# Performance work log

Measured on AMD Instinct MI355X. Metric: run time of the kernel, lower is better.

Reference implementation:

```python
import jax, jax.numpy as jnp
import numpy as np

B, S, D_IN, H = 64, 512, 2, 512


def lstm_cell(x, h, c, Wih, Whh, b):
    # PyTorch nn.LSTM gate layout: [i, f, g, o] stacked along rows of W (4H x in)
    gates = x @ Wih.T + h @ Whh.T + b  # [B, 4H]
    i, f, g, o = jnp.split(gates, 4, axis=-1)
    c = jax.nn.sigmoid(f) * c + jax.nn.sigmoid(i) * jnp.tanh(g)
    h = jax.nn.sigmoid(o) * jnp.tanh(c)
    return h, c


def setup_inputs() -> dict:
    key = jax.random.key(0)
    ks = jax.random.split(key, 12)
    s = 1.0 / np.sqrt(H)  # torch default uniform init scale
    u = lambda k, shape: jax.random.uniform(k, shape, jnp.float32, -s, s)
    return {
        "inputs": jax.random.normal(ks[0], (B, S, D_IN), jnp.float32),
        "enc_Wih": u(ks[1], (4 * H, D_IN)),
        "enc_Whh": u(ks[2], (4 * H, H)),
        "enc_bih": u(ks[3], (4 * H,)),
        "enc_bhh": u(ks[4], (4 * H,)),
        "dec_Wih": u(ks[5], (4 * H, H)),
        "dec_Whh": u(ks[6], (4 * H, H)),
        "dec_bih": u(ks[7], (4 * H,)),
        "dec_bhh": u(ks[8], (4 * H,)),
        "W_key": u(ks[9], (H, H)),
        "W_query": u(ks[10], (H, H)),
        "v": u(ks[11], (H,)),
        "max_output_len": S,
    }


def reference(inputs, enc_Wih, enc_Whh, enc_bih, enc_bhh,
              dec_Wih, dec_Whh, dec_bih, dec_bhh,
              W_key, W_query, v, max_output_len):
    batch, seq_len, _ = inputs.shape
    hid = W_key.shape[0]
    dtype = inputs.dtype

    # ---- Encoder LSTM over the sequence ----
    enc_b = enc_bih + enc_bhh
    h0 = jnp.zeros((batch, hid), dtype)

    def enc_step(carry, x_t):
        h, c = carry
        h, c = lstm_cell(x_t, h, c, enc_Wih, enc_Whh, enc_b)
        return (h, c), h

    (h, c), enc_outs = jax.lax.scan(enc_step, (h0, h0), jnp.swapaxes(inputs, 0, 1))
    enc_outs = jnp.swapaxes(enc_outs, 0, 1)  # [B, S, H]

    # keys are recomputed each step in the torch code but are step-invariant
    keys = enc_outs @ W_key.T  # [B, S, H]
    dec_b = dec_bih + dec_bhh

    # ---- Decoder loop with Bahdanau pointer attention ----
    def dec_step(carry, _):
        h_d, c_d, x = carry
        h_d, c_d = lstm_cell(x, h_d, c_d, dec_Wih, dec_Whh, dec_b)
        query = h_d @ W_query.T                                # [B, H]
        scores = jnp.tanh(query[:, None, :] + keys) @ v        # [B, S]
        probs = jax.nn.softmax(scores, axis=-1)
        context = jnp.einsum('bs,bsh->bh', probs, enc_outs)    # [B, H]
        return (h_d, c_d, context), scores

    x0 = jnp.zeros((batch, hid), dtype)
    _, all_scores = jax.lax.scan(dec_step, (h, c, x0), None, length=max_output_len)
    return jnp.swapaxes(all_scores, 0, 1)  # [B, T, S]
```

## Files before the change

kernel.cpp:

```cpp
#include <hip/hip_runtime.h>

constexpr int kNB = 64;
constexpr int kNS = 512;
constexpr int kNH = 512;
constexpr int kNG = 2048;
constexpr int kNT = 512;

__device__ __forceinline__ float chpn_sigmoid(float x) {
    return 1.0f / (1.0f + __expf(-x));
}
__device__ __forceinline__ float chpn_tanh(float x) {
    x = fmaxf(fminf(x, 15.0f), -15.0f);
    float e = __expf(2.0f * x);
    return (e - 1.0f) / (e + 1.0f);
}

__global__ void ConvexHullPointerNetwork_57303453663418_kernel(
    const float* ebih, const float* ebhh,
    const float* dbih, const float* dbhh,
    const float* wq,
    float* enc_b, float* dec_b, float* wqT, float* h0c)
{
    int i = blockIdx.x * 256 + threadIdx.x;
    if (i < kNG) { enc_b[i] = ebih[i] + ebhh[i]; dec_b[i] = dbih[i] + dbhh[i]; }
    if (i < 2 * kNB * kNH) h0c[i] = 0.0f;
    if (i < kNH * kNH) {
        int r = i >> 9, c = i & 511;
        wqT[c * kNH + r] = wq[i];
    }
}

__global__ __launch_bounds__(256) void chpn_enc_cell(
    const float* __restrict__ inputs, const float* __restrict__ wih,
    const float* __restrict__ whh, const float* __restrict__ bias,
    const float* __restrict__ h_src, float* __restrict__ h_dst,
    float* __restrict__ c_st, float* __restrict__ enc_outs, int t)
{
    __shared__ float tile[64][65];
    __shared__ float gate_lds[4][64];
    const int tid = threadIdx.x;
    const int bb = tid & 63, gg = tid >> 6;
    const int j = (int)blockIdx.x;

    const int r = gg * kNH + j;
    const float* w = whh + (size_t)r * kNH;
    float acc = 0.f;

    for (int ch = 0; ch < 8; ++ch) {
        const int k0 = ch * 64;
        for (int i = 0; i < 16; ++i) {
            int e = tid + i * 256; int kk = e & 63, b2 = e >> 6;
            tile[kk][b2] = h_src[b2 * kNH + k0 + kk];
        }
        __syncthreads();
        #pragma unroll
        for (int kk = 0; kk < 64; ++kk)
            acc = fmaf(tile[kk][bb], w[k0 + kk], acc);
        __syncthreads();
    }
    float x0 = inputs[(bb * kNS + t) * 2 + 0];
    float x1 = inputs[(bb * kNS + t) * 2 + 1];
    acc += bias[r] + wih[r * 2] * x0 + wih[r * 2 + 1] * x1;

    gate_lds[gg][bb] = acc;
    __syncthreads();
    if (tid < 64) {
        float gi = gate_lds[0][tid], gf = gate_lds[1][tid];
        float gc = gate_lds[2][tid], go = gate_lds[3][tid];
        float cc = chpn_sigmoid(gf) * c_st[tid * kNH + j] + chpn_sigmoid(gi) * chpn_tanh(gc);
        float hh = chpn_sigmoid(go) * chpn_tanh(cc);
        c_st[tid * kNH + j] = cc;
        h_dst[tid * kNH + j] = hh;
        enc_outs[((size_t)tid * kNS + t) * kNH + j] = hh;
    }
}

__global__ __launch_bounds__(256) void chpn_keys_gemm(
    const float* __restrict__ enc_outs, const float* __restrict__ wk,
    float* __restrict__ keysT)
{
    int bid = blockIdx.x;
    int bb = bid >> 6, ht = (bid >> 3) & 7, st = bid & 7;
    __shared__ float asb[32][66];
    __shared__ float bsb[32][66];
    int tid = threadIdx.x;
    int tx = tid & 15, ty = tid >> 4;
    float acc[4][4] = {};
    for (int j0 = 0; j0 < kNH; j0 += 32) {
        for (int i = 0; i < 8; ++i) {
            int e = tid + i * 256;
            int j = e & 31, s = e >> 5;
            asb[j][s] = enc_outs[((size_t)bb * kNS + st * 64 + s) * kNH + j0 + j];
            bsb[j][s] = wk[(size_t)(ht * 64 + s) * kNH + j0 + j];
        }
        __syncthreads();
        #pragma unroll 8
        for (int j = 0; j < 32; ++j) {
            float a0 = asb[j][tx*4], a1 = asb[j][tx*4+1], a2 = asb[j][tx*4+2], a3 = asb[j][tx*4+3];
            float b0 = bsb[j][ty*4], b1 = bsb[j][ty*4+1], b2 = bsb[j][ty*4+2], b3 = bsb[j][ty*4+3];
            acc[0][0] = fmaf(b0,a0,acc[0][0]); acc[0][1] = fmaf(b0,a1,acc[0][1]);
            acc[0][2] = fmaf(b0,a2,acc[0][2]); acc[0][3] = fmaf(b0,a3,acc[0][3]);
            acc[1][0] = fmaf(b1,a0,acc[1][0]); acc[1][1] = fmaf(b1,a1,acc[1][1]);
            acc[1][2] = fmaf(b1,a2,acc[1][2]); acc[1][3] = fmaf(b1,a3,acc[1][3]);
            acc[2][0] = fmaf(b2,a0,acc[2][0]); acc[2][1] = fmaf(b2,a1,acc[2][1]);
            acc[2][2] = fmaf(b2,a2,acc[2][2]); acc[2][3] = fmaf(b2,a3,acc[2][3]);
            acc[3][0] = fmaf(b3,a0,acc[3][0]); acc[3][1] = fmaf(b3,a1,acc[3][1]);
            acc[3][2] = fmaf(b3,a2,acc[3][2]); acc[3][3] = fmaf(b3,a3,acc[3][3]);
        }
        __syncthreads();
    }
    for (int i = 0; i < 4; ++i)
        for (int k = 0; k < 4; ++k)
            keysT[((size_t)bb * kNH + ht * 64 + ty * 4 + i) * kNS + st * 64 + tx * 4 + k] =
                acc[i][k];
}

__global__ __launch_bounds__(256) void chpn_dec_cell(
    const float* __restrict__ wih, const float* __restrict__ whh,
    const float* __restrict__ bias,
    const float* __restrict__ h_src, float* __restrict__ h_dst,
    float* __restrict__ c_st,
    const float* __restrict__ ctx_num, const float* __restrict__ denom,
    int first)
{
    __shared__ float tile[64][65];
    __shared__ float gate_lds[4][64];
    __shared__ float invd[64];
    const int tid = threadIdx.x;
    const int bb = tid & 63, gg = tid >> 6;
    const int j = (int)blockIdx.x;
    if (tid < 64) invd[tid] = first ? 0.0f : (1.0f / denom[tid]);
    __syncthreads();

    const int r = gg * kNH + j;
    float acc = 0.f;
    {
        const float* w = wih + (size_t)r * kNH;
        for (int ch = 0; ch < 8; ++ch) {
            const int k0 = ch * 64;
            for (int i = 0; i < 16; ++i) {
                int e = tid + i * 256; int kk = e & 63, b2 = e >> 6;
                tile[kk][b2] = first ? 0.0f : ctx_num[b2 * kNH + k0 + kk] * invd[b2];
            }
            __syncthreads();
            #pragma unroll
            for (int kk = 0; kk < 64; ++kk)
                acc = fmaf(tile[kk][bb], w[k0 + kk], acc);
            __syncthreads();
        }
    }
    {
        const float* w = whh + (size_t)r * kNH;
        for (int ch = 0; ch < 8; ++ch) {
            const int k0 = ch * 64;
            for (int i = 0; i < 16; ++i) {
                int e = tid + i * 256; int kk = e & 63, b2 = e >> 6;
                tile[kk][b2] = h_src[b2 * kNH + k0 + kk];
            }
            __syncthreads();
            #pragma unroll
            for (int kk = 0; kk < 64; ++kk)
                acc = fmaf(tile[kk][bb], w[k0 + kk], acc);
            __syncthreads();
        }
    }
    acc += bias[r];
    gate_lds[gg][bb] = acc;
    __syncthreads();
    if (tid < 64) {
        float gi = gate_lds[0][tid], gf = gate_lds[1][tid];
        float gc = gate_lds[2][tid], go = gate_lds[3][tid];
        float cc = chpn_sigmoid(gf) * c_st[tid * kNH + j] + chpn_sigmoid(gi) * chpn_tanh(gc);
        float hh = chpn_sigmoid(go) * chpn_tanh(cc);
        c_st[tid * kNH + j] = cc;
        h_dst[tid * kNH + j] = hh;
    }
}

__global__ __launch_bounds__(256) void chpn_query(
    const float* __restrict__ wqT, const float* __restrict__ h_src,
    float* __restrict__ query, float* __restrict__ ctx_num,
    float* __restrict__ denom)
{
    __shared__ float hl[kNH];
    __shared__ float part[256];
    int bid = blockIdx.x;
    int bb = bid >> 2, hc = bid & 3;
    int tid = threadIdx.x;
    int hl_idx = tid;
    hl[hl_idx] = h_src[bb * kNH + hl_idx];
    hl[hl_idx + 256] = h_src[bb * kNH + hl_idx + 256];
    __syncthreads();

    int h = hc * 128 + (tid & 127);
    int jh = tid >> 7;
    float acc = 0.f;
    const float* wcol = wqT + h;
    #pragma unroll 8
    for (int j = jh * 256; j < jh * 256 + 256; ++j)
        acc = fmaf(hl[j], wcol[(size_t)j * kNH], acc);
    part[tid] = acc;
    __syncthreads();
    if (tid < 128) {
        float q = part[tid] + part[tid + 128];
        query[bb * kNH + h] = q;
        ctx_num[bb * kNH + h] = 0.0f;
        if (hc == 0 && tid == 0) denom[bb] = 0.0f;
    }
}

__global__ __launch_bounds__(1024) void chpn_score_ctx(
    const float* __restrict__ keysT, const float* __restrict__ enc_outs,
    const float* __restrict__ query, const float* __restrict__ vvec,
    float* __restrict__ ctx_num, float* __restrict__ denom,
    float* __restrict__ out, int t)
{
    __shared__ float ql[kNH], vl[kNH];
    __shared__ float part[16][64];
    __shared__ float el[64];
    int bid = blockIdx.x;
    int bb = bid >> 3, sc = bid & 7;
    int s0 = sc * 64;
    int tid = threadIdx.x;
    int s = tid & 63, hq = tid >> 6;

    if (tid < kNH) { ql[tid] = query[bb * kNH + tid]; vl[tid] = vvec[tid]; }
    __syncthreads();

    float acc = 0.f;
    const float* kp = keysT + (size_t)bb * kNH * kNS + s0 + s;
    const int h0 = hq * 32;
    #pragma unroll 4
    for (int h = h0; h < h0 + 32; ++h) {
        float kv = kp[(size_t)h * kNS];
        acc = fmaf(vl[h], chpn_tanh(ql[h] + kv), acc);
    }
    part[hq][s] = acc;
    __syncthreads();

    if (tid < 64) {
        float scv = 0.f;
        #pragma unroll
        for (int q = 0; q < 16; ++q) scv += part[q][tid];
        out[((size_t)bb * kNT + t) * kNS + s0 + tid] = scv;
        float e = __expf(scv);
        el[tid] = e;
        float wsum = e;
        #pragma unroll
        for (int off = 32; off > 0; off >>= 1) wsum += __shfl_down(wsum, off);
        if (tid == 0) atomicAdd(&denom[bb], wsum);
    }
    __syncthreads();

    int j = tid & 511, sh = tid >> 9;
    float a = 0.f;
    const float* ep = enc_outs + ((size_t)bb * kNS + s0 + sh * 32) * kNH + j;
    #pragma unroll 4
    for (int ss = 0; ss < 32; ++ss)
        a = fmaf(el[sh * 32 + ss], ep[(size_t)ss * kNH], a);
    atomicAdd(&ctx_num[bb * kNH + j], a);
}

extern "C" void kernel_launch(void* const* d_in, const int* in_sizes, int n_in,
                              void* d_out, int out_size, void* d_ws, size_t ws_size,
                              hipStream_t stream) {
    const float* inputs = (const float*)d_in[0];
    const float* e_wih  = (const float*)d_in[1];
    const float* e_whh  = (const float*)d_in[2];
    const float* e_bih  = (const float*)d_in[3];
    const float* e_bhh  = (const float*)d_in[4];
    const float* d_wih  = (const float*)d_in[5];
    const float* d_whh  = (const float*)d_in[6];
    const float* d_bih  = (const float*)d_in[7];
    const float* d_bhh  = (const float*)d_in[8];
    const float* w_key  = (const float*)d_in[9];
    const float* w_qry  = (const float*)d_in[10];
    const float* v_vec  = (const float*)d_in[11];
    float* out = (float*)d_out;

    float* wsf   = (float*)d_ws;
    float* h0    = wsf;
    float* cst   = h0 + kNB * kNH;
    float* h1    = cst + kNB * kNH;
    float* query = h1 + kNB * kNH;
    float* ctxn  = query + kNB * kNH;
    float* denom = ctxn + kNB * kNH;
    float* encb  = denom + 64;
    float* decb  = encb + kNG;
    float* wqT   = decb + kNG;
    float* keysF = wqT + (size_t)kNH * kNH;
    float* encF  = keysF + (size_t)kNB * kNH * kNS;

    ConvexHullPointerNetwork_57303453663418_kernel<<<1024, 256, 0, stream>>>(
        e_bih, e_bhh, d_bih, d_bhh, w_qry, encb, decb, wqT, h0);

    for (int t = 0; t < kNS; ++t) {
        float* hs = (t & 1) ? h1 : h0;
        float* hd = (t & 1) ? h0 : h1;
        chpn_enc_cell<<<512, 256, 0, stream>>>(inputs, e_wih, e_whh, encb,
                                               hs, hd, cst, encF, t);
    }

    chpn_keys_gemm<<<4096, 256, 0, stream>>>(encF, w_key, keysF);

    for (int t = 0; t < kNT; ++t) {
        float* hs = (t & 1) ? h1 : h0;
        float* hd = (t & 1) ? h0 : h1;
        chpn_dec_cell<<<512, 256, 0, stream>>>(d_wih, d_whh, decb,
                                               hs, hd, cst,
                                               ctxn, denom, t == 0 ? 1 : 0);
        chpn_query<<<256, 256, 0, stream>>>(wqT, hd, query, ctxn, denom);
        chpn_score_ctx<<<512, 1024, 0, stream>>>(keysF, encF, query, v_vec,
                                                 ctxn, denom, out, t);
    }
}
```

Before: 70.88 ms.

## Replace per-step kernel launches with persistent cooperative kernels using grid sync

Encoder and decoder recurrences now each run as a single cooperative persistent kernel of 256 blocks x 512 threads. Each block handles two hidden units, and steps are separated by grid.sync() instead of about 2000 separate kernel launches. The decoder fuses the LSTM cell, query projection and score/context stages into one loop with three grid barriers per step. Score and context work is remapped to 128-position chunks per block. This removes launch overhead but lowers parallelism per stage (256 blocks instead of 512 for the attention step) and adds grid-wide barrier cost. The old multi-launch path is kept as a fallback if the cooperative launch fails.

```diff
diff --git a/kernel.cpp b/kernel.cpp
--- a/kernel.cpp
+++ b/kernel.cpp
@@ -1,4 +1,7 @@
 #include <hip/hip_runtime.h>
+#include <hip/hip_cooperative_groups.h>
+
+namespace cg = cooperative_groups;
 
 constexpr int kNB = 64;
 constexpr int kNS = 512;
@@ -30,7 +33,205 @@
     }
 }
 
-__global__ __launch_bounds__(256) void chpn_enc_cell(
+__global__ __launch_bounds__(512) void chpn_enc_loop(
+    const float* __restrict__ inputs, const float* __restrict__ wih,
+    const float* __restrict__ whh, const float* __restrict__ bias,
+    float* __restrict__ h0, float* __restrict__ h1,
+    float* __restrict__ c_st, float* __restrict__ enc_outs)
+{
+    cg::grid_group grid = cg::this_grid();
+    __shared__ float tile[64][65];
+    __shared__ float gate_lds[2][4][64];
+    const int tid = threadIdx.x;
+    const int bb = tid & 63, gg = (tid >> 6) & 3, jj = tid >> 8;
+    const int j = (int)blockIdx.x * 2 + jj;
+    const int r = gg * kNH + j;
+    const float* w = whh + (size_t)r * kNH;
+    const float wx0 = wih[r * 2], wx1 = wih[r * 2 + 1], bj = bias[r];
+
+    for (int t = 0; t < kNS; ++t) {
+        const float* hs = (t & 1) ? h1 : h0;
+        float* hd = (t & 1) ? h0 : h1;
+        float acc = 0.f;
+        for (int ch = 0; ch < 8; ++ch) {
+            const int k0 = ch * 64;
+            for (int i = 0; i < 8; ++i) {
+                int e = tid + i * 512; int kk = e & 63, b2 = e >> 6;
+                tile[kk][b2] = hs[b2 * kNH + k0 + kk];
+            }
+            __syncthreads();
+            #pragma unroll
+            for (int kk = 0; kk < 64; ++kk)
+                acc = fmaf(tile[kk][bb], w[k0 + kk], acc);
+            __syncthreads();
+        }
+        float x0 = inputs[(bb * kNS + t) * 2 + 0];
+        float x1 = inputs[(bb * kNS + t) * 2 + 1];
+        acc += bj + wx0 * x0 + wx1 * x1;
+        gate_lds[jj][gg][bb] = acc;
+        __syncthreads();
+        if (tid < 128) {
+            int j2 = (int)blockIdx.x * 2 + (tid >> 6), b = tid & 63;
+            int jl = tid >> 6;
+            float gi = gate_lds[jl][0][b], gf = gate_lds[jl][1][b];
+            float gc = gate_lds[jl][2][b], go = gate_lds[jl][3][b];
+            float cc = chpn_sigmoid(gf) * c_st[b * kNH + j2] +
+                       chpn_sigmoid(gi) * chpn_tanh(gc);
+            float hh = chpn_sigmoid(go) * chpn_tanh(cc);
+            c_st[b * kNH + j2] = cc;
+            hd[b * kNH + j2] = hh;
+            enc_outs[((size_t)b * kNS + t) * kNH + j2] = hh;
+        }
+        __syncthreads();
+        grid.sync();
+    }
+}
+
+__global__ __launch_bounds__(512) void chpn_dec_loop(
+    const float* __restrict__ wih, const float* __restrict__ whh,
+    const float* __restrict__ bias, const float* __restrict__ wqT,
+    const float* __restrict__ vvec,
+    const float* __restrict__ keysT, const float* __restrict__ enc_outs,
+    float* __restrict__ h0, float* __restrict__ h1, float* __restrict__ c_st,
+    float* __restrict__ query, float* __restrict__ ctx_num,
+    float* __restrict__ denom, float* __restrict__ out)
+{
+    cg::grid_group grid = cg::this_grid();
+    __shared__ float tile[64][65];
+    __shared__ float gate_lds[2][4][64];
+    __shared__ float invd[64];
+    __shared__ float qpart[4][128];
+    __shared__ float ql[kNH], vl[kNH];
+    __shared__ float part[4][128];
+    __shared__ float el[128];
+
+    const int tid = threadIdx.x;
+    const int bid = (int)blockIdx.x;
+    const int bb = tid & 63, gg = (tid >> 6) & 3, jj = tid >> 8;
+    const int j = bid * 2 + jj;
+    const int rr = gg * kNH + j;
+    const float* wih_r = wih + (size_t)rr * kNH;
+    const float* whh_r = whh + (size_t)rr * kNH;
+    const float bias_r = bias[rr];
+    const int qb = bid >> 2, qc = bid & 3;
+    const int s0 = qc * 128;
+
+    for (int t = 0; t < kNT; ++t) {
+        const int first = (t == 0);
+        const float* hs = (t & 1) ? h1 : h0;
+        float* hd = (t & 1) ? h0 : h1;
+
+        if (tid < 64) invd[tid] = first ? 0.0f : (1.0f / denom[tid]);
+        __syncthreads();
+        float acc = 0.f;
+        for (int ch = 0; ch < 8; ++ch) {
+            const int k0 = ch * 64;
+            for (int i = 0; i < 8; ++i) {
+                int e = tid + i * 512; int kk = e & 63, b2 = e >> 6;
+                tile[kk][b2] = first ? 0.0f
+                             : ctx_num[b2 * kNH + k0 + kk] * invd[b2];
+            }
+            __syncthreads();
+            #pragma unroll
+            for (int kk = 0; kk < 64; ++kk)
+                acc = fmaf(tile[kk][bb], wih_r[k0 + kk], acc);
+            __syncthreads();
+        }
+        for (int ch = 0; ch < 8; ++ch) {
+            const int k0 = ch * 64;
+            for (int i = 0; i < 8; ++i) {
+                int e = tid + i * 512; int kk = e & 63, b2 = e >> 6;
+                tile[kk][b2] = hs[b2 * kNH + k0 + kk];
+            }
+            __syncthreads();
+            #pragma unroll
+            for (int kk = 0; kk < 64; ++kk)
+                acc = fmaf(tile[kk][bb], whh_r[k0 + kk], acc);
+            __syncthreads();
+        }
+        acc += bias_r;
+        gate_lds[jj][gg][bb] = acc;
+        __syncthreads();
+        if (tid < 128) {
+            int j2 = bid * 2 + (tid >> 6), b = tid & 63;
+            int jl = tid >> 6;
+            float gi = gate_lds[jl][0][b], gf = gate_lds[jl][1][b];
+            float gc = gate_lds[jl][2][b], go = gate_lds[jl][3][b];
+            float cc = chpn_sigmoid(gf) * c_st[b * kNH + j2] +
+                       chpn_sigmoid(gi) * chpn_tanh(gc);
+            float hh = chpn_sigmoid(go) * chpn_tanh(cc);
+            c_st[b * kNH + j2] = cc;
+            hd[b * kNH + j2] = hh;
+        }
+        __syncthreads();
+        grid.sync();
+
+        {
+            int h = qc * 128 + (tid & 127);
+            int jq = tid >> 7;
+            float qa = 0.f;
+            const float* wcol = wqT + h;
+            const float* hb = hd + qb * kNH;
+            #pragma unroll 8
+            for (int jx = jq * 128; jx < jq * 128 + 128; ++jx)
+                qa = fmaf(hb[jx], wcol[(size_t)jx * kNH], qa);
+            qpart[jq][tid & 127] = qa;
+            __syncthreads();
+            if (tid < 128) {
+                float q = qpart[0][tid] + qpart[1][tid] +
+                          qpart[2][tid] + qpart[3][tid];
+                query[qb * kNH + qc * 128 + tid] = q;
+                ctx_num[qb * kNH + qc * 128 + tid] = 0.0f;
+                if (qc == 0 && tid == 0) denom[qb] = 0.0f;
+            }
+            __syncthreads();
+        }
+        grid.sync();
+
+        {
+            ql[tid] = query[qb * kNH + tid];
+            vl[tid] = vvec[tid];
+            __syncthreads();
+
+            int s = tid & 127, hq = tid >> 7;
+            float sa = 0.f;
+            const float* kp = keysT + (size_t)qb * kNH * kNS + s0 + s;
+            const int h0i = hq * 128;
+            #pragma unroll 4
+            for (int h = h0i; h < h0i + 128; ++h) {
+                float kv = kp[(size_t)h * kNS];
+                sa = fmaf(vl[h], chpn_tanh(ql[h] + kv), sa);
+            }
+            part[hq][s] = sa;
+            __syncthreads();
+
+            if (tid < 128) {
+                float scv = part[0][tid] + part[1][tid] +
+                            part[2][tid] + part[3][tid];
+                out[((size_t)qb * kNT + t) * kNS + s0 + tid] = scv;
+                float e = __expf(scv);
+                el[tid] = e;
+                float wsum = e;
+                #pragma unroll
+                for (int off = 32; off > 0; off >>= 1)
+                    wsum += __shfl_down(wsum, off);
+                if ((tid & 63) == 0) atomicAdd(&denom[qb], wsum);
+            }
+            __syncthreads();
+
+            float a = 0.f;
+            const float* ep = enc_outs + ((size_t)qb * kNS + s0) * kNH + tid;
+            #pragma unroll 4
+            for (int ss = 0; ss < 128; ++ss)
+                a = fmaf(el[ss], ep[(size_t)ss * kNH], a);
+            atomicAdd(&ctx_num[qb * kNH + tid], a);
+            __syncthreads();
+        }
+        grid.sync();
+    }
+}
+
+__global__ __launch_bounds__(256) void fb_enc_cell(
     const float* __restrict__ inputs, const float* __restrict__ wih,
     const float* __restrict__ whh, const float* __restrict__ bias,
     const float* __restrict__ h_src, float* __restrict__ h_dst,
@@ -41,11 +242,9 @@
     const int tid = threadIdx.x;
     const int bb = tid & 63, gg = tid >> 6;
     const int j = (int)blockIdx.x;
-
     const int r = gg * kNH + j;
     const float* w = whh + (size_t)r * kNH;
     float acc = 0.f;
-
     for (int ch = 0; ch < 8; ++ch) {
         const int k0 = ch * 64;
         for (int i = 0; i < 16; ++i) {
@@ -61,7 +260,6 @@
     float x0 = inputs[(bb * kNS + t) * 2 + 0];
     float x1 = inputs[(bb * kNS + t) * 2 + 1];
     acc += bias[r] + wih[r * 2] * x0 + wih[r * 2 + 1] * x1;
-
     gate_lds[gg][bb] = acc;
     __syncthreads();
     if (tid < 64) {
@@ -73,6 +271,145 @@
         h_dst[tid * kNH + j] = hh;
         enc_outs[((size_t)tid * kNS + t) * kNH + j] = hh;
     }
+}
+
+__global__ __launch_bounds__(256) void fb_dec_cell(
+    const float* __restrict__ wih, const float* __restrict__ whh,
+    const float* __restrict__ bias,
+    const float* __restrict__ h_src, float* __restrict__ h_dst,
+    float* __restrict__ c_st,
+    const float* __restrict__ ctx_num, const float* __restrict__ denom,
+    int first)
+{
+    __shared__ float tile[64][65];
+    __shared__ float gate_lds[4][64];
+    __shared__ float invd[64];
+    const int tid = threadIdx.x;
+    const int bb = tid & 63, gg = tid >> 6;
+    const int j = (int)blockIdx.x;
+    if (tid < 64) invd[tid] = first ? 0.0f : (1.0f / denom[tid]);
+    __syncthreads();
+    const int r = gg * kNH + j;
+    float acc = 0.f;
+    {
+        const float* w = wih + (size_t)r * kNH;
+        for (int ch = 0; ch < 8; ++ch) {
+            const int k0 = ch * 64;
+            for (int i = 0; i < 16; ++i) {
+                int e = tid + i * 256; int kk = e & 63, b2 = e >> 6;
+                tile[kk][b2] = first ? 0.0f : ctx_num[b2 * kNH + k0 + kk] * invd[b2];
+            }
+            __syncthreads();
+            #pragma unroll
+            for (int kk = 0; kk < 64; ++kk)
+                acc = fmaf(tile[kk][bb], w[k0 + kk], acc);
+            __syncthreads();
+        }
+    }
+    {
+        const float* w = whh + (size_t)r * kNH;
+        for (int ch = 0; ch < 8; ++ch) {
+            const int k0 = ch * 64;
+            for (int i = 0; i < 16; ++i) {
+                int e = tid + i * 256; int kk = e & 63, b2 = e >> 6;
+                tile[kk][b2] = h_src[b2 * kNH + k0 + kk];
+            }
+            __syncthreads();
+            #pragma unroll
+            for (int kk = 0; kk < 64; ++kk)
+                acc = fmaf(tile[kk][bb], w[k0 + kk], acc);
+            __syncthreads();
+        }
+    }
+    acc += bias[r];
+    gate_lds[gg][bb] = acc;
+    __syncthreads();
+    if (tid < 64) {
+        float gi = gate_lds[0][tid], gf = gate_lds[1][tid];
+        float gc = gate_lds[2][tid], go = gate_lds[3][tid];
+        float cc = chpn_sigmoid(gf) * c_st[tid * kNH + j] + chpn_sigmoid(gi) * chpn_tanh(gc);
+        float hh = chpn_sigmoid(go) * chpn_tanh(cc);
+        c_st[tid * kNH + j] = cc;
+        h_dst[tid * kNH + j] = hh;
+    }
+}
+
+__global__ __launch_bounds__(256) void fb_query(
+    const float* __restrict__ wqT, const float* __restrict__ h_src,
+    float* __restrict__ query, float* __restrict__ ctx_num,
+    float* __restrict__ denom)
+{
+    __shared__ float hl[kNH];
+    __shared__ float partq[256];
+    int bid = blockIdx.x;
+    int bb = bid >> 2, hc = bid & 3;
+    int tid = threadIdx.x;
+    hl[tid] = h_src[bb * kNH + tid];
+    hl[tid + 256] = h_src[bb * kNH + tid + 256];
+    __syncthreads();
+    int h = hc * 128 + (tid & 127);
+    int jh = tid >> 7;
+    float acc = 0.f;
+    const float* wcol = wqT + h;
+    #pragma unroll 8
+    for (int j = jh * 256; j < jh * 256 + 256; ++j)
+        acc = fmaf(hl[j], wcol[(size_t)j * kNH], acc);
+    partq[tid] = acc;
+    __syncthreads();
+    if (tid < 128) {
+        float q = partq[tid] + partq[tid + 128];
+        query[bb * kNH + h] = q;
+        ctx_num[bb * kNH + h] = 0.0f;
+        if (hc == 0 && tid == 0) denom[bb] = 0.0f;
+    }
+}
+
+__global__ __launch_bounds__(1024) void fb_score_ctx(
+    const float* __restrict__ keysT, const float* __restrict__ enc_outs,
+    const float* __restrict__ query, const float* __restrict__ vvec,
+    float* __restrict__ ctx_num, float* __restrict__ denom,
+    float* __restrict__ out, int t)
+{
+    __shared__ float ql[kNH], vl[kNH];
+    __shared__ float part[16][64];
+    __shared__ float el[64];
+    int bid = blockIdx.x;
+    int bb = bid >> 3, sc = bid & 7;
+    int s0 = sc * 64;
+    int tid = threadIdx.x;
+    int s = tid & 63, hq = tid >> 6;
+    if (tid < kNH) { ql[tid] = query[bb * kNH + tid]; vl[tid] = vvec[tid]; }
+    __syncthreads();
+    float acc = 0.f;
+    const float* kp = keysT + (size_t)bb * kNH * kNS + s0 + s;
+    const int h0 = hq * 32;
+    #pragma unroll 4
+    for (int h = h0; h < h0 + 32; ++h) {
+        float kv = kp[(size_t)h * kNS];
+        acc = fmaf(vl[h], chpn_tanh(ql[h] + kv), acc);
+    }
+    part[hq][s] = acc;
+    __syncthreads();
+    if (tid < 64) {
+        float scv = 0.f;
+        #pragma unroll
+        for (int q = 0; q < 16; ++q) scv += part[q][tid];
+        out[((size_t)bb * kNT + t) * kNS + s0 + tid] = scv;
+        float e = __expf(scv);
+        el[tid] = e;
+        float wsum = e;
+        #pragma unroll
+        for (int off = 32; off > 0; off >>= 1) wsum += __shfl_down(wsum, off);
+        if (tid == 0) atomicAdd(&denom[bb], wsum);
+    }
+    __syncthreads();
+    int j = tid & 511, sh = tid >> 9;
+    float a = 0.f;
+    const float* ep = enc_outs + ((size_t)bb * kNS + s0 + sh * 32) * kNH + j;
+    #pragma unroll 4
+    for (int ss = 0; ss < 32; ++ss)
+        a = fmaf(el[sh * 32 + ss], ep[(size_t)ss * kNH], a);
+    atomicAdd(&ctx_num[bb * kNH + j], a);
 }
 
 __global__ __launch_bounds__(256) void chpn_keys_gemm(
@@ -113,152 +450,6 @@
         for (int k = 0; k < 4; ++k)
             keysT[((size_t)bb * kNH + ht * 64 + ty * 4 + i) * kNS + st * 64 + tx * 4 + k] =
                 acc[i][k];
-}
-
-__global__ __launch_bounds__(256) void chpn_dec_cell(
-    const float* __restrict__ wih, const float* __restrict__ whh,
-    const float* __restrict__ bias,
-    const float* __restrict__ h_src, float* __restrict__ h_dst,
-    float* __restrict__ c_st,
-    const float* __restrict__ ctx_num, const float* __restrict__ denom,
-    int first)
-{
-    __shared__ float tile[64][65];
-    __shared__ float gate_lds[4][64];
-    __shared__ float invd[64];
-    const int tid = threadIdx.x;
-    const int bb = tid & 63, gg = tid >> 6;
-    const int j = (int)blockIdx.x;
-    if (tid < 64) invd[tid] = first ? 0.0f : (1.0f / denom[tid]);
-    __syncthreads();
-
-    const int r = gg * kNH + j;
-    float acc = 0.f;
-    {
-        const float* w = wih + (size_t)r * kNH;
-        for (int ch = 0; ch < 8; ++ch) {
-            const int k0 = ch * 64;
-            for (int i = 0; i < 16; ++i) {
-                int e = tid + i * 256; int kk = e & 63, b2 = e >> 6;
-                tile[kk][b2] = first ? 0.0f : ctx_num[b2 * kNH + k0 + kk] * invd[b2];
-            }
-            __syncthreads();
-            #pragma unroll
-            for (int kk = 0; kk < 64; ++kk)
-                acc = fmaf(tile[kk][bb], w[k0 + kk], acc);
-            __syncthreads();
-        }
-    }
-    {
-        const float* w = whh + (size_t)r * kNH;
-        for (int ch = 0; ch < 8; ++ch) {
-            const int k0 = ch * 64;
-            for (int i = 0; i < 16; ++i) {
-                int e = tid + i * 256; int kk = e & 63, b2 = e >> 6;
-                tile[kk][b2] = h_src[b2 * kNH + k0 + kk];
-            }
-            __syncthreads();
-            #pragma unroll
-            for (int kk = 0; kk < 64; ++kk)
-                acc = fmaf(tile[kk][bb], w[k0 + kk], acc);
-            __syncthreads();
-        }
-    }
-    acc += bias[r];
-    gate_lds[gg][bb] = acc;
-    __syncthreads();
-    if (tid < 64) {
-        float gi = gate_lds[0][tid], gf = gate_lds[1][tid];
-        float gc = gate_lds[2][tid], go = gate_lds[3][tid];
-        float cc = chpn_sigmoid(gf) * c_st[tid * kNH + j] + chpn_sigmoid(gi) * chpn_tanh(gc);
-        float hh = chpn_sigmoid(go) * chpn_tanh(cc);
-        c_st[tid * kNH + j] = cc;
-        h_dst[tid * kNH + j] = hh;
-    }
-}
-
-__global__ __launch_bounds__(256) void chpn_query(
-    const float* __restrict__ wqT, const float* __restrict__ h_src,
-    float* __restrict__ query, float* __restrict__ ctx_num,
-    float* __restrict__ denom)
-{
-    __shared__ float hl[kNH];
-    __shared__ float part[256];
-    int bid = blockIdx.x;
-    int bb = bid >> 2, hc = bid & 3;
-    int tid = threadIdx.x;
-    int hl_idx = tid;
-    hl[hl_idx] = h_src[bb * kNH + hl_idx];
-    hl[hl_idx + 256] = h_src[bb * kNH + hl_idx + 256];
-    __syncthreads();
-
-    int h = hc * 128 + (tid & 127);
-    int jh = tid >> 7;
-    float acc = 0.f;
-    const float* wcol = wqT + h;
-    #pragma unroll 8
-    for (int j = jh * 256; j < jh * 256 + 256; ++j)
-        acc = fmaf(hl[j], wcol[(size_t)j * kNH], acc);
-    part[tid] = acc;
-    __syncthreads();
-    if (tid < 128) {
-        float q = part[tid] + part[tid + 128];
-        query[bb * kNH + h] = q;
-        ctx_num[bb * kNH + h] = 0.0f;
-        if (hc == 0 && tid == 0) denom[bb] = 0.0f;
-    }
-}
-
-__global__ __launch_bounds__(1024) void chpn_score_ctx(
-    const float* __restrict__ keysT, const float* __restrict__ enc_outs,
-    const float* __restrict__ query, const float* __restrict__ vvec,
-    float* __restrict__ ctx_num, float* __restrict__ denom,
-    float* __restrict__ out, int t)
-{
-    __shared__ float ql[kNH], vl[kNH];
-    __shared__ float part[16][64];
-    __shared__ float el[64];
-    int bid = blockIdx.x;
-    int bb = bid >> 3, sc = bid & 7;
-    int s0 = sc * 64;
-    int tid = threadIdx.x;
-    int s = tid & 63, hq = tid >> 6;
-
-    if (tid < kNH) { ql[tid] = query[bb * kNH + tid]; vl[tid] = vvec[tid]; }
-    __syncthreads();
-
-    float acc = 0.f;
-    const float* kp = keysT + (size_t)bb * kNH * kNS + s0 + s;
-    const int h0 = hq * 32;
-    #pragma unroll 4
-    for (int h = h0; h < h0 + 32; ++h) {
-        float kv = kp[(size_t)h * kNS];
-        acc = fmaf(vl[h], chpn_tanh(ql[h] + kv), acc);
-    }
-    part[hq][s] = acc;
-    __syncthreads();
-
-    if (tid < 64) {
-        float scv = 0.f;
-        #pragma unroll
-        for (int q = 0; q < 16; ++q) scv += part[q][tid];
-        out[((size_t)bb * kNT + t) * kNS + s0 + tid] = scv;
-        float e = __expf(scv);
-        el[tid] = e;
-        float wsum = e;
-        #pragma unroll
-        for (int off = 32; off > 0; off >>= 1) wsum += __shfl_down(wsum, off);
-        if (tid == 0) atomicAdd(&denom[bb], wsum);
-    }
-    __syncthreads();
-
-    int j = tid & 511, sh = tid >> 9;
-    float a = 0.f;
-    const float* ep = enc_outs + ((size_t)bb * kNS + s0 + sh * 32) * kNH + j;
-    #pragma unroll 4
-    for (int ss = 0; ss < 32; ++ss)
-        a = fmaf(el[sh * 32 + ss], ep[(size_t)ss * kNH], a);
-    atomicAdd(&ctx_num[bb * kNH + j], a);
 }
 
 extern "C" void kernel_launch(void* const* d_in, const int* in_sizes, int n_in,
@@ -294,23 +485,47 @@
     ConvexHullPointerNetwork_57303453663418_kernel<<<1024, 256, 0, stream>>>(
         e_bih, e_bhh, d_bih, d_bhh, w_qry, encb, decb, wqT, h0);
 
-    for (int t = 0; t < kNS; ++t) {
-        float* hs = (t & 1) ? h1 : h0;
-        float* hd = (t & 1) ? h0 : h1;
-        chpn_enc_cell<<<512, 256, 0, stream>>>(inputs, e_wih, e_whh, encb,
-                                               hs, hd, cst, encF, t);
+    {
+        void* args[] = { (void*)&inputs, (void*)&e_wih, (void*)&e_whh,
+                         (void*)&encb, (void*)&h0, (void*)&h1,
+                         (void*)&cst, (void*)&encF };
+        hipError_t rc = hipLaunchCooperativeKernel((const void*)chpn_enc_loop,
+                                                   dim3(256), dim3(512),
+                                                   args, 0, stream);
+        if (rc != hipSuccess) {
+            (void)hipGetLastError();
+            for (int t = 0; t < kNS; ++t) {
+                float* hs = (t & 1) ? h1 : h0;
+                float* hd = (t & 1) ? h0 : h1;
+                fb_enc_cell<<<512, 256, 0, stream>>>(inputs, e_wih, e_whh, encb,
+                                                     hs, hd, cst, encF, t);
+            }
+        }
     }
 
     chpn_keys_gemm<<<4096, 256, 0, stream>>>(encF, w_key, keysF);
 
-    for (int t = 0; t < kNT; ++t) {
-        float* hs = (t & 1) ? h1 : h0;
-        float* hd = (t & 1) ? h0 : h1;
-        chpn_dec_cell<<<512, 256, 0, stream>>>(d_wih, d_whh, decb,
-                                               hs, hd, cst,
-                                               ctxn, denom, t == 0 ? 1 : 0);
-        chpn_query<<<256, 256, 0, stream>>>(wqT, hd, query, ctxn, denom);
-        chpn_score_ctx<<<512, 1024, 0, stream>>>(keysF, encF, query, v_vec,
-                                                 ctxn, denom, out, t);
-    }
-}
+    {
+        void* args[] = { (void*)&d_wih, (void*)&d_whh, (void*)&decb,
+                         (void*)&wqT, (void*)&v_vec, (void*)&keysF,
+                         (void*)&encF, (void*)&h0, (void*)&h1, (void*)&cst,
+                         (void*)&query, (void*)&ctxn, (void*)&denom,
+                         (void*)&out };
+        hipError_t rc = hipLaunchCooperativeKernel((const void*)chpn_dec_loop,
+                                                   dim3(256), dim3(512),
+                                                   args, 0, stream);
+        if (rc != hipSuccess) {
+            (void)hipGetLastError();
+            for (int t = 0; t < kNT; ++t) {
+                float* hs = (t & 1) ? h1 : h0;
+                float* hd = (t & 1) ? h0 : h1;
+                fb_dec_cell<<<512, 256, 0, stream>>>(d_wih, d_whh, decb,
+                                                     hs, hd, cst,
+                                                     ctxn, denom, t == 0 ? 1 : 0);
+                fb_query<<<256, 256, 0, stream>>>(wqT, hd, query, ctxn, denom);
+                fb_score_ctx<<<512, 1024, 0, stream>>>(keysF, encF, query, v_vec,
+                                                       ctxn, denom, out, t);
+            }
+        }
+    }
+}
```

Result: slower. 127.8 ms (+80.3%).

## Store encoder outputs and keys in fp16 and restructure query projection

Applied to the files above, without the earlier changes.

Encoder outputs and the precomputed attention keys are now stored as _Float16 instead of float. This halves the memory traffic of the per-step score/context kernel, which streams keys and encoder outputs for the whole batch every decoder step. The query projection is also rewritten to read W_query rows directly, with an LDS-staged hidden tile shared across the batch, so the W_query transpose in the setup kernel is dropped. The cost is reduced precision in the keys and encoder outputs, which feed the output scores and the context vector.

```diff
diff --git a/kernel.cpp b/kernel.cpp
--- a/kernel.cpp
+++ b/kernel.cpp
@@ -6,6 +6,8 @@
 constexpr int kNG = 2048;
 constexpr int kNT = 512;
 
+typedef _Float16 chpn_f16;
+
 __device__ __forceinline__ float chpn_sigmoid(float x) {
     return 1.0f / (1.0f + __expf(-x));
 }
@@ -18,34 +20,27 @@
 __global__ void ConvexHullPointerNetwork_57303453663418_kernel(
     const float* ebih, const float* ebhh,
     const float* dbih, const float* dbhh,
-    const float* wq,
-    float* enc_b, float* dec_b, float* wqT, float* h0c)
+    float* enc_b, float* dec_b, float* h0c)
 {
     int i = blockIdx.x * 256 + threadIdx.x;
     if (i < kNG) { enc_b[i] = ebih[i] + ebhh[i]; dec_b[i] = dbih[i] + dbhh[i]; }
     if (i < 2 * kNB * kNH) h0c[i] = 0.0f;
-    if (i < kNH * kNH) {
-        int r = i >> 9, c = i & 511;
-        wqT[c * kNH + r] = wq[i];
-    }
 }
 
 __global__ __launch_bounds__(256) void chpn_enc_cell(
     const float* __restrict__ inputs, const float* __restrict__ wih,
     const float* __restrict__ whh, const float* __restrict__ bias,
     const float* __restrict__ h_src, float* __restrict__ h_dst,
-    float* __restrict__ c_st, float* __restrict__ enc_outs, int t)
+    float* __restrict__ c_st, chpn_f16* __restrict__ enc_outs, int t)
 {
     __shared__ float tile[64][65];
     __shared__ float gate_lds[4][64];
     const int tid = threadIdx.x;
     const int bb = tid & 63, gg = tid >> 6;
     const int j = (int)blockIdx.x;
-
     const int r = gg * kNH + j;
     const float* w = whh + (size_t)r * kNH;
     float acc = 0.f;
-
     for (int ch = 0; ch < 8; ++ch) {
         const int k0 = ch * 64;
         for (int i = 0; i < 16; ++i) {
@@ -61,7 +56,6 @@
     float x0 = inputs[(bb * kNS + t) * 2 + 0];
     float x1 = inputs[(bb * kNS + t) * 2 + 1];
     acc += bias[r] + wih[r * 2] * x0 + wih[r * 2 + 1] * x1;
-
     gate_lds[gg][bb] = acc;
     __syncthreads();
     if (tid < 64) {
@@ -71,13 +65,13 @@
         float hh = chpn_sigmoid(go) * chpn_tanh(cc);
         c_st[tid * kNH + j] = cc;
         h_dst[tid * kNH + j] = hh;
-        enc_outs[((size_t)tid * kNS + t) * kNH + j] = hh;
+        enc_outs[((size_t)tid * kNS + t) * kNH + j] = (chpn_f16)hh;
     }
 }
 
 __global__ __launch_bounds__(256) void chpn_keys_gemm(
-    const float* __restrict__ enc_outs, const float* __restrict__ wk,
-    float* __restrict__ keysT)
+    const chpn_f16* __restrict__ enc_outs, const float* __restrict__ wk,
+    chpn_f16* __restrict__ keysT)
 {
     int bid = blockIdx.x;
     int bb = bid >> 6, ht = (bid >> 3) & 7, st = bid & 7;
@@ -90,7 +84,7 @@
         for (int i = 0; i < 8; ++i) {
             int e = tid + i * 256;
             int j = e & 31, s = e >> 5;
-            asb[j][s] = enc_outs[((size_t)bb * kNS + st * 64 + s) * kNH + j0 + j];
+            asb[j][s] = (float)enc_outs[((size_t)bb * kNS + st * 64 + s) * kNH + j0 + j];
             bsb[j][s] = wk[(size_t)(ht * 64 + s) * kNH + j0 + j];
         }
         __syncthreads();
@@ -112,7 +106,7 @@
     for (int i = 0; i < 4; ++i)
         for (int k = 0; k < 4; ++k)
             keysT[((size_t)bb * kNH + ht * 64 + ty * 4 + i) * kNS + st * 64 + tx * 4 + k] =
-                acc[i][k];
+                (chpn_f16)acc[i][k];
 }
 
 __global__ __launch_bounds__(256) void chpn_dec_cell(
@@ -131,7 +125,6 @@
     const int j = (int)blockIdx.x;
     if (tid < 64) invd[tid] = first ? 0.0f : (1.0f / denom[tid]);
     __syncthreads();
-
     const int r = gg * kNH + j;
     float acc = 0.f;
     {
@@ -177,40 +170,51 @@
     }
 }
 
-__global__ __launch_bounds__(256) void chpn_query(
-    const float* __restrict__ wqT, const float* __restrict__ h_src,
+__global__ __launch_bounds__(256) void chpn_query_ws(
+    const float* __restrict__ wq, const float* __restrict__ h_src,
     float* __restrict__ query, float* __restrict__ ctx_num,
     float* __restrict__ denom)
 {
-    __shared__ float hl[kNH];
-    __shared__ float part[256];
-    int bid = blockIdx.x;
-    int bb = bid >> 2, hc = bid & 3;
-    int tid = threadIdx.x;
-    int hl_idx = tid;
-    hl[hl_idx] = h_src[bb * kNH + hl_idx];
-    hl[hl_idx + 256] = h_src[bb * kNH + hl_idx + 256];
-    __syncthreads();
-
-    int h = hc * 128 + (tid & 127);
-    int jh = tid >> 7;
-    float acc = 0.f;
-    const float* wcol = wqT + h;
-    #pragma unroll 8
-    for (int j = jh * 256; j < jh * 256 + 256; ++j)
-        acc = fmaf(hl[j], wcol[(size_t)j * kNH], acc);
-    part[tid] = acc;
+    __shared__ float tile[128][65];
+    __shared__ float qp[4][2][64];
+    const int tid = threadIdx.x;
+    const int bb = tid & 63, p = tid >> 6;
+    const int h0 = (int)blockIdx.x * 2;
+    const float* w0 = wq + (size_t)h0 * kNH;
+    const float* w1 = w0 + kNH;
+
+    float a0 = 0.f, a1 = 0.f;
+    for (int ch = 0; ch < 4; ++ch) {
+        const int j0 = ch * 128;
+        for (int i = 0; i < 32; ++i) {
+            int e = tid + i * 256; int jj = e & 127, b2 = e >> 7;
+            tile[jj][b2] = h_src[b2 * kNH + j0 + jj];
+        }
+        __syncthreads();
+        if (ch == p) {
+            #pragma unroll 4
+            for (int jj = 0; jj < 128; ++jj) {
+                float hv = tile[jj][bb];
+                a0 = fmaf(hv, w0[j0 + jj], a0);
+                a1 = fmaf(hv, w1[j0 + jj], a1);
+            }
+        }
+        __syncthreads();
+    }
+    qp[p][0][bb] = a0;
+    qp[p][1][bb] = a1;
     __syncthreads();
     if (tid < 128) {
-        float q = part[tid] + part[tid + 128];
-        query[bb * kNH + h] = q;
-        ctx_num[bb * kNH + h] = 0.0f;
-        if (hc == 0 && tid == 0) denom[bb] = 0.0f;
+        int b2 = tid & 63, hh = tid >> 6;
+        float q = qp[0][hh][b2] + qp[1][hh][b2] + qp[2][hh][b2] + qp[3][hh][b2];
+        query[b2 * kNH + h0 + hh] = q;
+        ctx_num[b2 * kNH + h0 + hh] = 0.0f;
+        if (blockIdx.x == 0 && hh == 0) denom[b2] = 0.0f;
     }
 }
 
 __global__ __launch_bounds__(1024) void chpn_score_ctx(
-    const float* __restrict__ keysT, const float* __restrict__ enc_outs,
+    const chpn_f16* __restrict__ keysT, const chpn_f16* __restrict__ enc_outs,
     const float* __restrict__ query, const float* __restrict__ vvec,
     float* __restrict__ ctx_num, float* __restrict__ denom,
     float* __restrict__ out, int t)
@@ -223,21 +227,18 @@
     int s0 = sc * 64;
     int tid = threadIdx.x;
     int s = tid & 63, hq = tid >> 6;
-
     if (tid < kNH) { ql[tid] = query[bb * kNH + tid]; vl[tid] = vvec[tid]; }
     __syncthreads();
-
     float acc = 0.f;
-    const float* kp = keysT + (size_t)bb * kNH * kNS + s0 + s;
+    const chpn_f16* kp = keysT + (size_t)bb * kNH * kNS + s0 + s;
     const int h0 = hq * 32;
     #pragma unroll 4
     for (int h = h0; h < h0 + 32; ++h) {
-        float kv = kp[(size_t)h * kNS];
+        float kv = (float)kp[(size_t)h * kNS];
         acc = fmaf(vl[h], chpn_tanh(ql[h] + kv), acc);
     }
     part[hq][s] = acc;
     __syncthreads();
-
     if (tid < 64) {
         float scv = 0.f;
         #pragma unroll
@@ -251,13 +252,12 @@
         if (tid == 0) atomicAdd(&denom[bb], wsum);
     }
     __syncthreads();
-
     int j = tid & 511, sh = tid >> 9;
     float a = 0.f;
-    const float* ep = enc_outs + ((size_t)bb * kNS + s0 + sh * 32) * kNH + j;
+    const chpn_f16* ep = enc_outs + ((size_t)bb * kNS + s0 + sh * 32) * kNH + j;
     #pragma unroll 4
     for (int ss = 0; ss < 32; ++ss)
-        a = fmaf(el[sh * 32 + ss], ep[(size_t)ss * kNH], a);
+        a = fmaf(el[sh * 32 + ss], (float)ep[(size_t)ss * kNH], a);
     atomicAdd(&ctx_num[bb * kNH + j], a);
 }
 
@@ -287,21 +287,20 @@
     float* denom = ctxn + kNB * kNH;
     float* encb  = denom + 64;
     float* decb  = encb + kNG;
-    float* wqT   = decb + kNG;
-    float* keysF = wqT + (size_t)kNH * kNH;
-    float* encF  = keysF + (size_t)kNB * kNH * kNS;
-
-    ConvexHullPointerNetwork_57303453663418_kernel<<<1024, 256, 0, stream>>>(
-        e_bih, e_bhh, d_bih, d_bhh, w_qry, encb, decb, wqT, h0);
+    chpn_f16* keysH = (chpn_f16*)(decb + kNG);
+    chpn_f16* encH  = keysH + (size_t)kNB * kNH * kNS;
+
+    ConvexHullPointerNetwork_57303453663418_kernel<<<256, 256, 0, stream>>>(
+        e_bih, e_bhh, d_bih, d_bhh, encb, decb, h0);
 
     for (int t = 0; t < kNS; ++t) {
         float* hs = (t & 1) ? h1 : h0;
         float* hd = (t & 1) ? h0 : h1;
         chpn_enc_cell<<<512, 256, 0, stream>>>(inputs, e_wih, e_whh, encb,
-                                               hs, hd, cst, encF, t);
-    }
-
-    chpn_keys_gemm<<<4096, 256, 0, stream>>>(encF, w_key, keysF);
+                                               hs, hd, cst, encH, t);
+    }
+
+    chpn_keys_gemm<<<4096, 256, 0, stream>>>(encH, w_key, keysH);
 
     for (int t = 0; t < kNT; ++t) {
         float* hs = (t & 1) ? h1 : h0;
@@ -309,8 +308,8 @@
         chpn_dec_cell<<<512, 256, 0, stream>>>(d_wih, d_whh, decb,
                                                hs, hd, cst,
                                                ctxn, denom, t == 0 ? 1 : 0);
-        chpn_query<<<256, 256, 0, stream>>>(wqT, hd, query, ctxn, denom);
-        chpn_score_ctx<<<512, 1024, 0, stream>>>(keysF, encF, query, v_vec,
+        chpn_query_ws<<<256, 256, 0, stream>>>(w_qry, hd, query, ctxn, denom);
+        chpn_score_ctx<<<512, 1024, 0, stream>>>(keysH, encH, query, v_vec,
                                                  ctxn, denom, out, t);
     }
 }
```

New measurement: 73.68 ms. +3.9%, slower.
